# Performance work log

Measured on AMD Instinct MI355X. Metric: run time of the kernel, lower is better.

The kernel has to match this reference:

```python
import jax, jax.numpy as jnp
import numpy as np

BLOCK_DIM = 32
INPUT_DIM = 1024
N_BLOCKS = INPUT_DIM // BLOCK_DIM  # 32
HIDDEN = 2 * BLOCK_DIM             # 64
GAPS = [1, 32]                     # block_dim**i for i in range(num_layers=2)


def setup_inputs() -> dict:
    key = jax.random.key(0)
    ks = jax.random.split(key, 9)
    s = 1.0 / np.sqrt(BLOCK_DIM)
    sh = 1.0 / np.sqrt(HIDDEN)
    return {
        "x": jax.random.normal(ks[0], (16384, INPUT_DIM), dtype=jnp.float32),
        # facto net 0: BlockLinear(32, 32, 64) -> ELU -> BlockLinear(32, 64, 32)
        "W1a": jax.random.uniform(ks[1], (N_BLOCKS, BLOCK_DIM, HIDDEN), jnp.float32, -s, s),
        "b1a": jax.random.uniform(ks[2], (N_BLOCKS, HIDDEN), jnp.float32, -s, s),
        "W2a": jax.random.uniform(ks[3], (N_BLOCKS, HIDDEN, BLOCK_DIM), jnp.float32, -sh, sh),
        "b2a": jax.random.uniform(ks[4], (N_BLOCKS, BLOCK_DIM), jnp.float32, -sh, sh),
        # facto net 1
        "W1b": jax.random.uniform(ks[5], (N_BLOCKS, BLOCK_DIM, HIDDEN), jnp.float32, -s, s),
        "b1b": jax.random.uniform(ks[6], (N_BLOCKS, HIDDEN), jnp.float32, -s, s),
        "W2b": jax.random.uniform(ks[7], (N_BLOCKS, HIDDEN, BLOCK_DIM), jnp.float32, -sh, sh),
        "b2b": jax.random.uniform(ks[8], (N_BLOCKS, BLOCK_DIM), jnp.float32, -sh, sh),
    }


def _block_res_mlp(x, W1, b1, W2, b2):
    # x: (bs, input_dim) -> (n_blocks, bs, block_dim)
    bs = x.shape[0]
    xb = x.reshape(bs, N_BLOCKS, BLOCK_DIM).transpose(1, 0, 2)
    h = jax.nn.elu(jnp.einsum('nbi,nio->nbo', xb, W1) + b1[:, None, :])
    h = jnp.einsum('nbi,nio->nbo', h, W2) + b2[:, None, :]
    yb = h + xb  # residual
    return yb.transpose(1, 0, 2).reshape(bs, -1)


def reference(x, W1a, b1a, W2a, b2a, W1b, b1b, W2b, b2b):
    bs = x.shape[0]
    params = [(W1a, b1a, W2a, b2a), (W1b, b1b, W2b, b2b)]
    y = x
    for gap, (W1, b1, W2, b2) in zip(GAPS, params):
        # strided mixing permutation before the block MLP
        y = y.reshape(-1, BLOCK_DIM, gap).transpose(0, 2, 1).reshape(bs, -1)
        y = _block_res_mlp(y, W1, b1, W2, b2)
        # inverse permutation
        y = y.reshape(-1, gap, BLOCK_DIM).transpose(0, 2, 1)
    return y.reshape(bs, -1)
```

## Files before the change

kernel.cpp:

```cpp
#include <hip/hip_runtime.h>


typedef unsigned short u16t;
typedef __bf16 bf16x8 __attribute__((ext_vector_type(8)));
typedef float f32x4 __attribute__((ext_vector_type(4)));

#define TILE_LD 1032
#define HT_LD   20

__device__ __forceinline__ u16t f2b(float f) {
  union { float f; unsigned u; } v; v.f = f;
  unsigned r = v.u + 0x7FFFu + ((v.u >> 16) & 1u);
  return (u16t)(r >> 16);
}
__device__ __forceinline__ float b2f(u16t h) {
  union { unsigned u; float f; } v; v.u = ((unsigned)h) << 16;
  return v.f;
}

__global__ __launch_bounds__(256) void pack_weights(
    const float* __restrict__ W1a, const float* __restrict__ W2a,
    const float* __restrict__ W1b, const float* __restrict__ W2b,
    u16t* __restrict__ pW1, u16t* __restrict__ pW2) {
  int tidg = blockIdx.x * 256 + threadIdx.x;
  int tensor = tidg >> 14;
  int r  = tidg & 16383;
  int L  = r >> 13;
  int r2 = r & 8191;
  int n    = r2 >> 8;
  int f    = (r2 >> 6) & 3;
  int lane = r2 & 63;
  int q = lane >> 4, t = lane & 15;

  union { u16t us[8]; uint4 v; } w;
  if (tensor == 0) {
    const float* src = L ? W1b : W1a;
#pragma unroll
    for (int j = 0; j < 8; j++)
      w.us[j] = f2b(src[n * 2048 + (q * 8 + j) * 64 + f * 16 + t]);
    *(uint4*)(pW1 + (size_t)((((L * 32 + n) * 4 + f) * 64 + lane) * 8)) = w.v;
  } else {
    const float* src = L ? W2b : W2a;
    int kc = f >> 1, c2 = f & 1;
#pragma unroll
    for (int j = 0; j < 8; j++)
      w.us[j] = f2b(src[n * 2048 + (kc * 32 + q * 8 + j) * 32 + c2 * 16 + t]);
    *(uint4*)(pW2 + (size_t)((((L * 32 + n) * 4 + f) * 64 + lane) * 8)) = w.v;
  }
}

struct Frags {
  bf16x8 w1[4];
  bf16x8 w2[4];
  float  b1v[4];
  float  b2v[2];
};

__device__ __forceinline__ void load_frags(Frags& F, int L, int n, int lane, int t,
    const u16t* __restrict__ pW1, const u16t* __restrict__ pW2,
    const float* __restrict__ b1, const float* __restrict__ b2) {
  const int base = ((L * 32 + n) * 4) * 512 + lane * 8;
#pragma unroll
  for (int f = 0; f < 4; f++) {
    F.w1[f] = *(const bf16x8*)(pW1 + base + f * 512);
    F.w2[f] = *(const bf16x8*)(pW2 + base + f * 512);
  }
#pragma unroll
  for (int c = 0; c < 4; c++) F.b1v[c] = b1[n * 64 + c * 16 + t];
  F.b2v[0] = b2[n * 32 + t];
  F.b2v[1] = b2[n * 32 + 16 + t];
}

template <int L>
__device__ __forceinline__ void compute_layer(
    const bf16x8* afr, u16t* __restrict__ tile, u16t* __restrict__ hT,
    const u16t* __restrict__ pW1, const u16t* __restrict__ pW2,
    const float* __restrict__ b1, const float* __restrict__ b2,
    int wave, int lane, int q, int t, const bf16x8* ifr) {
  const f32x4 zf = {0.f, 0.f, 0.f, 0.f};
  Frags cur, nxt;
  load_frags(cur, L, wave * 8, lane, t, pW1, pW2, b1, b2);
#pragma unroll
  for (int u = 0; u < 8; u++) {
    const int n = wave * 8 + u;
    if (u < 7) load_frags(nxt, L, n + 1, lane, t, pW1, pW2, b1, b2);

    f32x4 accH[4];
#pragma unroll
    for (int c = 0; c < 4; c++)
      accH[c] = __builtin_amdgcn_mfma_f32_16x16x32_bf16(afr[u], cur.w1[c], zf, 0, 0, 0);

#pragma unroll
    for (int c = 0; c < 4; c++) {
      union { u16t us[4]; ushort4 v; } hw;
#pragma unroll
      for (int r = 0; r < 4; r++) {
        float v = accH[c][r] + cur.b1v[c];
        v = v > 0.f ? v : (__expf(v) - 1.f);
        hw.us[r] = f2b(v);
      }
      *(ushort4*)(hT + (c * 16 + t) * HT_LD + 4 * q) = hw.v;
    }

    union { u16t us[8]; bf16x8 v; } a0, a1;
#pragma unroll
    for (int j = 0; j < 8; j++) {
      a0.us[j] = hT[(q * 8 + j) * HT_LD + t];
      a1.us[j] = hT[(32 + q * 8 + j) * HT_LD + t];
    }

#pragma unroll
    for (int c2 = 0; c2 < 2; c2++) {
      f32x4 acc = __builtin_amdgcn_mfma_f32_16x16x32_bf16(afr[u], ifr[c2], zf, 0, 0, 0);
      acc = __builtin_amdgcn_mfma_f32_16x16x32_bf16(a0.v, cur.w2[c2],     acc, 0, 0, 0);
      acc = __builtin_amdgcn_mfma_f32_16x16x32_bf16(a1.v, cur.w2[2 + c2], acc, 0, 0, 0);
#pragma unroll
      for (int r = 0; r < 4; r++) {
        float v = acc[r] + cur.b2v[c2];
        int row = q * 4 + r;
        int cc  = c2 * 16 + t;
        int phys;
        if (L == 0) phys = n * 32 + (cc ^ ((((n >> 3) & 3)) << 1));
        else        phys = (cc * 32 + n) ^ ((cc & 7) << 3);
        tile[row * TILE_LD + phys] = f2b(v);
      }
    }
    cur = nxt;
  }
}

__global__ __launch_bounds__(256) void mixer_kernel(
    const float* __restrict__ x,
    const float* __restrict__ b1a, const float* __restrict__ b2a,
    const float* __restrict__ b1b, const float* __restrict__ b2b,
    const u16t* __restrict__ pW1, const u16t* __restrict__ pW2,
    float* __restrict__ out) {
  __shared__ u16t tile[16 * TILE_LD];
  __shared__ u16t hT[4][64 * HT_LD];

  const int tid  = threadIdx.x;
  const int wave = tid >> 6, lane = tid & 63;
  const int q = lane >> 4, t = lane & 15;
  const int r0 = blockIdx.x * 16;

  bf16x8 ifr[2];
#pragma unroll
  for (int c2 = 0; c2 < 2; c2++) {
    union { u16t us[8]; bf16x8 v; } w;
#pragma unroll
    for (int j = 0; j < 8; j++)
      w.us[j] = ((q * 8 + j) == (c2 * 16 + t)) ? (u16t)0x3F80 : (u16t)0;
    ifr[c2] = w.v;
  }

  bf16x8 afr[8];
#pragma unroll
  for (int u = 0; u < 8; u++) {
    const int n = wave * 8 + u;
    const float* gp = x + (size_t)(r0 + t) * 1024 + n * 32 + q * 8;
    float4 v0 = *(const float4*)gp;
    float4 v1 = *(const float4*)(gp + 4);
    union { u16t us[8]; bf16x8 v; } a;
    a.us[0] = f2b(v0.x); a.us[1] = f2b(v0.y); a.us[2] = f2b(v0.z); a.us[3] = f2b(v0.w);
    a.us[4] = f2b(v1.x); a.us[5] = f2b(v1.y); a.us[6] = f2b(v1.z); a.us[7] = f2b(v1.w);
    afr[u] = a.v;
  }
  compute_layer<0>(afr, tile, hT[wave], pW1, pW2, b1a, b2a, wave, lane, q, t, ifr);
  __syncthreads();

#pragma unroll
  for (int u = 0; u < 8; u++) {
    const int n2 = wave * 8 + u;
    const int nx = n2 ^ (q << 1);
    union { u16t us[8]; bf16x8 v; } a;
#pragma unroll
    for (int j = 0; j < 8; j++)
      a.us[j] = tile[t * TILE_LD + (q * 8 + j) * 32 + nx];
    afr[u] = a.v;
  }
  __syncthreads();
  compute_layer<1>(afr, tile, hT[wave], pW1, pW2, b1b, b2b, wave, lane, q, t, ifr);
  __syncthreads();

#pragma unroll
  for (int i = 0; i < 16; i++) {
    int e = i * 256 + tid;
    int row = e >> 8, g = e & 255;
    int C = 4 * g;
    int phys = C ^ (((g >> 3) & 7) << 3);
    ushort4 hv = *(const ushort4*)(tile + row * TILE_LD + phys);
    float4 o;
    o.x = b2f(hv.x); o.y = b2f(hv.y); o.z = b2f(hv.z); o.w = b2f(hv.w);
    *(float4*)(out + (size_t)(r0 + row) * 1024 + C) = o;
  }
}

extern "C" void kernel_launch(void* const* d_in, const int* in_sizes, int n_in,
                              void* d_out, int out_size, void* d_ws, size_t ws_size,
                              hipStream_t stream) {
  const float* x   = (const float*)d_in[0];
  const float* W1a = (const float*)d_in[1];
  const float* b1a = (const float*)d_in[2];
  const float* W2a = (const float*)d_in[3];
  const float* b2a = (const float*)d_in[4];
  const float* W1b = (const float*)d_in[5];
  const float* b1b = (const float*)d_in[6];
  const float* W2b = (const float*)d_in[7];
  const float* b2b = (const float*)d_in[8];
  float* out = (float*)d_out;

  u16t* pW1 = (u16t*)d_ws;
  u16t* pW2 = pW1 + 131072;

  const int rows = in_sizes[0] / 1024;

  pack_weights<<<128, 256, 0, stream>>>(W1a, W2a, W1b, W2b, pW1, pW2);
  mixer_kernel<<<rows / 16, 256, 0, stream>>>(x, b1a, b2a, b1b, b2b, pW1, pW2, out);
}
```

Before: 158.1 us.

## Transpose MFMA operand roles to keep hidden activations in registers

```diff
diff --git a/kernel.cpp b/kernel.cpp
--- a/kernel.cpp
+++ b/kernel.cpp
@@ -5,8 +5,7 @@
 typedef __bf16 bf16x8 __attribute__((ext_vector_type(8)));
 typedef float f32x4 __attribute__((ext_vector_type(4)));
 
-#define TILE_LD 1032
-#define HT_LD   20
+#define LDC 34
 
 __device__ __forceinline__ u16t f2b(float f) {
   union { float f; unsigned u; } v; v.f = f;
@@ -17,6 +16,8 @@
   union { unsigned u; float f; } v; v.u = ((unsigned)h) << 16;
   return v.f;
 }
+
+union BF { u16t us[8]; bf16x8 v; };
 
 __global__ __launch_bounds__(256) void pack_weights(
     const float* __restrict__ W1a, const float* __restrict__ W2a,
@@ -36,162 +37,154 @@
   if (tensor == 0) {
     const float* src = L ? W1b : W1a;
 #pragma unroll
-    for (int j = 0; j < 8; j++)
-      w.us[j] = f2b(src[n * 2048 + (q * 8 + j) * 64 + f * 16 + t]);
-    *(uint4*)(pW1 + (size_t)((((L * 32 + n) * 4 + f) * 64 + lane) * 8)) = w.v;
+    for (int j = 0; j < 8; j++) {
+      int kz = L ? (4 * j + q) : (q * 8 + j);
+      w.us[j] = f2b(src[n * 2048 + kz * 64 + f * 16 + t]);
+    }
+    *(uint4*)(pW1 + (size_t)((L * 32 + n) * 2048 + f * 512 + lane * 8)) = w.v;
   } else {
     const float* src = L ? W2b : W2a;
     int kc = f >> 1, c2 = f & 1;
 #pragma unroll
-    for (int j = 0; j < 8; j++)
-      w.us[j] = f2b(src[n * 2048 + (kc * 32 + q * 8 + j) * 32 + c2 * 16 + t]);
-    *(uint4*)(pW2 + (size_t)((((L * 32 + n) * 4 + f) * 64 + lane) * 8)) = w.v;
-  }
-}
-
-struct Frags {
-  bf16x8 w1[4];
-  bf16x8 w2[4];
-  float  b1v[4];
-  float  b2v[2];
-};
-
-__device__ __forceinline__ void load_frags(Frags& F, int L, int n, int lane, int t,
-    const u16t* __restrict__ pW1, const u16t* __restrict__ pW2,
-    const float* __restrict__ b1, const float* __restrict__ b2) {
-  const int base = ((L * 32 + n) * 4) * 512 + lane * 8;
-#pragma unroll
-  for (int f = 0; f < 4; f++) {
-    F.w1[f] = *(const bf16x8*)(pW1 + base + f * 512);
-    F.w2[f] = *(const bf16x8*)(pW2 + base + f * 512);
-  }
-#pragma unroll
-  for (int c = 0; c < 4; c++) F.b1v[c] = b1[n * 64 + c * 16 + t];
-  F.b2v[0] = b2[n * 32 + t];
-  F.b2v[1] = b2[n * 32 + 16 + t];
+    for (int j = 0; j < 8; j++) {
+      int H = kc * 32 + (j >> 2) * 16 + q * 4 + (j & 3);
+      w.us[j] = f2b(src[n * 2048 + H * 32 + c2 * 16 + t]);
+    }
+    *(uint4*)(pW2 + (size_t)((L * 32 + n) * 2048 + f * 512 + lane * 8)) = w.v;
+  }
 }
 
 template <int L>
 __device__ __forceinline__ void compute_layer(
-    const bf16x8* afr, u16t* __restrict__ tile, u16t* __restrict__ hT,
+    const bf16x8* afr, unsigned* __restrict__ tile32,
     const u16t* __restrict__ pW1, const u16t* __restrict__ pW2,
     const float* __restrict__ b1, const float* __restrict__ b2,
-    int wave, int lane, int q, int t, const bf16x8* ifr) {
+    const bf16x8* E, int w, int q, int t, int lane) {
   const f32x4 zf = {0.f, 0.f, 0.f, 0.f};
-  Frags cur, nxt;
-  load_frags(cur, L, wave * 8, lane, t, pW1, pW2, b1, b2);
 #pragma unroll
   for (int u = 0; u < 8; u++) {
-    const int n = wave * 8 + u;
-    if (u < 7) load_frags(nxt, L, n + 1, lane, t, pW1, pW2, b1, b2);
-
+    const int n = w * 8 + u;
+    const int base = (L * 32 + n) * 2048 + lane * 8;
+    bf16x8 w1f[4], w2f[4];
+#pragma unroll
+    for (int c = 0; c < 4; c++) {
+      w1f[c] = *(const bf16x8*)(pW1 + base + c * 512);
+      w2f[c] = *(const bf16x8*)(pW2 + base + c * 512);
+    }
     f32x4 accH[4];
 #pragma unroll
     for (int c = 0; c < 4; c++)
-      accH[c] = __builtin_amdgcn_mfma_f32_16x16x32_bf16(afr[u], cur.w1[c], zf, 0, 0, 0);
-
+      accH[c] = __builtin_amdgcn_mfma_f32_16x16x32_bf16(w1f[c], afr[u], zf, 0, 0, 0);
+
+    BF hf[2];
 #pragma unroll
     for (int c = 0; c < 4; c++) {
-      union { u16t us[4]; ushort4 v; } hw;
+      union { float4 v; float f[4]; } B1;
+      B1.v = *(const float4*)(b1 + n * 64 + c * 16 + q * 4);
 #pragma unroll
       for (int r = 0; r < 4; r++) {
-        float v = accH[c][r] + cur.b1v[c];
-        v = v > 0.f ? v : (__expf(v) - 1.f);
-        hw.us[r] = f2b(v);
+        float vv = accH[c][r] + B1.f[r];
+        vv = vv > 0.f ? vv : (__expf(vv) - 1.f);
+        hf[c >> 1].us[(c & 1) * 4 + r] = f2b(vv);
       }
-      *(ushort4*)(hT + (c * 16 + t) * HT_LD + 4 * q) = hw.v;
-    }
-
-    union { u16t us[8]; bf16x8 v; } a0, a1;
-#pragma unroll
-    for (int j = 0; j < 8; j++) {
-      a0.us[j] = hT[(q * 8 + j) * HT_LD + t];
-      a1.us[j] = hT[(32 + q * 8 + j) * HT_LD + t];
     }
 
 #pragma unroll
     for (int c2 = 0; c2 < 2; c2++) {
-      f32x4 acc = __builtin_amdgcn_mfma_f32_16x16x32_bf16(afr[u], ifr[c2], zf, 0, 0, 0);
-      acc = __builtin_amdgcn_mfma_f32_16x16x32_bf16(a0.v, cur.w2[c2],     acc, 0, 0, 0);
-      acc = __builtin_amdgcn_mfma_f32_16x16x32_bf16(a1.v, cur.w2[2 + c2], acc, 0, 0, 0);
-#pragma unroll
-      for (int r = 0; r < 4; r++) {
-        float v = acc[r] + cur.b2v[c2];
-        int row = q * 4 + r;
-        int cc  = c2 * 16 + t;
-        int phys;
-        if (L == 0) phys = n * 32 + (cc ^ ((((n >> 3) & 3)) << 1));
-        else        phys = (cc * 32 + n) ^ ((cc & 7) << 3);
-        tile[row * TILE_LD + phys] = f2b(v);
-      }
-    }
-    cur = nxt;
-  }
-}
-
-__global__ __launch_bounds__(256) void mixer_kernel(
+      f32x4 acc = __builtin_amdgcn_mfma_f32_16x16x32_bf16(E[c2], afr[u], zf, 0, 0, 0);
+      acc = __builtin_amdgcn_mfma_f32_16x16x32_bf16(w2f[c2],     hf[0].v, acc, 0, 0, 0);
+      acc = __builtin_amdgcn_mfma_f32_16x16x32_bf16(w2f[2 + c2], hf[1].v, acc, 0, 0, 0);
+      union { float4 v; float f[4]; } B2;
+      B2.v = *(const float4*)(b2 + n * 32 + c2 * 16 + q * 4);
+      const int phys = ((c2 * 16 + q * 4) + 4 * (n >> 2)) & 31;
+      const int a32 = (((n * 16 + t) * LDC) + phys) >> 1;
+      unsigned d0 = (unsigned)f2b(acc[0] + B2.f[0]) | ((unsigned)f2b(acc[1] + B2.f[1]) << 16);
+      unsigned d1 = (unsigned)f2b(acc[2] + B2.f[2]) | ((unsigned)f2b(acc[3] + B2.f[3]) << 16);
+      tile32[a32] = d0;
+      tile32[a32 + 1] = d1;
+    }
+  }
+}
+
+__global__ __launch_bounds__(256, 4) void mixer_kernel(
     const float* __restrict__ x,
     const float* __restrict__ b1a, const float* __restrict__ b2a,
     const float* __restrict__ b1b, const float* __restrict__ b2b,
     const u16t* __restrict__ pW1, const u16t* __restrict__ pW2,
     float* __restrict__ out) {
-  __shared__ u16t tile[16 * TILE_LD];
-  __shared__ u16t hT[4][64 * HT_LD];
-
-  const int tid  = threadIdx.x;
-  const int wave = tid >> 6, lane = tid & 63;
+  __shared__ unsigned tile32[(32 * 16 * LDC) / 2];
+  const u16t* tile16 = (const u16t*)tile32;
+  const int tid = threadIdx.x, w = tid >> 6, lane = tid & 63;
   const int q = lane >> 4, t = lane & 15;
   const int r0 = blockIdx.x * 16;
 
-  bf16x8 ifr[2];
-#pragma unroll
-  for (int c2 = 0; c2 < 2; c2++) {
-    union { u16t us[8]; bf16x8 v; } w;
-#pragma unroll
-    for (int j = 0; j < 8; j++)
-      w.us[j] = ((q * 8 + j) == (c2 * 16 + t)) ? (u16t)0x3F80 : (u16t)0;
-    ifr[c2] = w.v;
-  }
-
   bf16x8 afr[8];
 #pragma unroll
   for (int u = 0; u < 8; u++) {
-    const int n = wave * 8 + u;
+    const int n = w * 8 + u;
     const float* gp = x + (size_t)(r0 + t) * 1024 + n * 32 + q * 8;
     float4 v0 = *(const float4*)gp;
     float4 v1 = *(const float4*)(gp + 4);
-    union { u16t us[8]; bf16x8 v; } a;
+    BF a;
     a.us[0] = f2b(v0.x); a.us[1] = f2b(v0.y); a.us[2] = f2b(v0.z); a.us[3] = f2b(v0.w);
     a.us[4] = f2b(v1.x); a.us[5] = f2b(v1.y); a.us[6] = f2b(v1.z); a.us[7] = f2b(v1.w);
     afr[u] = a.v;
   }
-  compute_layer<0>(afr, tile, hT[wave], pW1, pW2, b1a, b2a, wave, lane, q, t, ifr);
+
+  bf16x8 E[2];
+#pragma unroll
+  for (int c2 = 0; c2 < 2; c2++) {
+    BF e;
+#pragma unroll
+    for (int j = 0; j < 8; j++)
+      e.us[j] = (q * 8 + j == c2 * 16 + t) ? (u16t)0x3F80 : (u16t)0;
+    E[c2] = e.v;
+  }
+
+  compute_layer<0>(afr, tile32, pW1, pW2, b1a, b2a, E, w, q, t, lane);
   __syncthreads();
 
-#pragma unroll
-  for (int u = 0; u < 8; u++) {
-    const int n2 = wave * 8 + u;
-    const int nx = n2 ^ (q << 1);
-    union { u16t us[8]; bf16x8 v; } a;
+  BF zfr[8];
+#pragma unroll
+  for (int j = 0; j < 8; j++) {
+    const int k = 4 * j + q;
+    const int rb = (k * 16 + t) * LDC;
+#pragma unroll
+    for (int g = 0; g < 2; g++) {
+      const int pg = (8 * w + 4 * g + 4 * j) & 31;
+      const unsigned d0 = tile32[(rb + pg) >> 1];
+      const unsigned d1 = tile32[((rb + pg) >> 1) + 1];
+      zfr[4 * g + 0].us[j] = (u16t)(d0 & 0xFFFF);
+      zfr[4 * g + 1].us[j] = (u16t)(d0 >> 16);
+      zfr[4 * g + 2].us[j] = (u16t)(d1 & 0xFFFF);
+      zfr[4 * g + 3].us[j] = (u16t)(d1 >> 16);
+    }
+  }
+
+#pragma unroll
+  for (int c2 = 0; c2 < 2; c2++) {
+    BF e;
 #pragma unroll
     for (int j = 0; j < 8; j++)
-      a.us[j] = tile[t * TILE_LD + (q * 8 + j) * 32 + nx];
-    afr[u] = a.v;
+      e.us[j] = (4 * j + q == c2 * 16 + t) ? (u16t)0x3F80 : (u16t)0;
+    E[c2] = e.v;
   }
   __syncthreads();
-  compute_layer<1>(afr, tile, hT[wave], pW1, pW2, b1b, b2b, wave, lane, q, t, ifr);
+
+  compute_layer<1>((const bf16x8*)zfr, tile32, pW1, pW2, b1b, b2b, E, w, q, t, lane);
   __syncthreads();
 
+  const int row = lane & 15, l4 = lane >> 4;
 #pragma unroll
   for (int i = 0; i < 16; i++) {
-    int e = i * 256 + tid;
-    int row = e >> 8, g = e & 255;
-    int C = 4 * g;
-    int phys = C ^ (((g >> 3) & 7) << 3);
-    ushort4 hv = *(const ushort4*)(tile + row * TILE_LD + phys);
-    float4 o;
-    o.x = b2f(hv.x); o.y = b2f(hv.y); o.z = b2f(hv.z); o.w = b2f(hv.w);
-    *(float4*)(out + (size_t)(r0 + row) * 1024 + C) = o;
+    const int F0 = 4 * (i * 16 + w * 4 + l4);
+    const int bn = F0 & 31, cc = F0 >> 5;
+    const int phys = (cc + 4 * (bn >> 2)) & 31;
+    union { float4 v; float f[4]; } o;
+#pragma unroll
+    for (int e = 0; e < 4; e++)
+      o.f[e] = b2f(tile16[((bn + e) * 16 + row) * LDC + phys]);
+    *(float4*)(out + (size_t)(r0 + row) * 1024 + F0) = o.v;
   }
 }
 
```

New measurement: 180.5 us. +14.2%, slower.
